# Performance work log

Hardware: AMD Instinct MI355X
Metric: run time of the kernel (lower is better)

## Reference

```python
import jax, jax.numpy as jnp
import numpy as np

SPLIT_SHAPE = (16, 16, 16, 16)  # per-variable state counts; joint space = 65536
NUM_CLASSES = 100
STABLE = 1e-6


def setup_inputs() -> dict:
    key = jax.random.key(0)
    k1, k2 = jax.random.split(key)
    B = 1024
    logits = jax.random.normal(k1, (B, sum(SPLIT_SHAPE)), dtype=jnp.float32)
    labels = jax.random.randint(k2, (B,), 0, NUM_CLASSES)
    y_true = jax.nn.one_hot(labels, NUM_CLASSES, dtype=jnp.float32)
    return {"logits": logits, "y_true": y_true}


def reference(logits, y_true):
    B = logits.shape[0]
    # split logits into per-variable blocks and softmax each -> P(Ak|Xi)
    splits = np.cumsum(SPLIT_SHAPE)[:-1]
    variables = [jax.nn.softmax(p, axis=-1) for p in jnp.split(logits, splits, axis=-1)]
    # joint sample space via iterative outer products: [B, s1, ..., sN]
    joint = variables[0]
    for v in variables[1:]:
        joint = jnp.einsum('b...,ba->b...a', joint, v)
    flat = joint.reshape(B, -1)  # [B, J], J = prod(SPLIT_SHAPE)
    # observation: numerator/denominator counts (fresh recorder, first call)
    num_y_joint = jnp.einsum('bj,by->yj', flat, y_true)  # [Y, J]
    num_joint = jnp.sum(flat, axis=0)                     # [J]
    prob_y_joint = jnp.clip(
        jnp.maximum(num_y_joint, STABLE) / jnp.maximum(num_joint, STABLE), 0.0, 1.0)
    # inference: posterior P^A(Yi|Xi)
    probs = jnp.einsum('yj,bj->by', prob_y_joint, flat)  # [B, Y]
    return probs
```

## Files before the change

### kernel.cpp

```cpp
#include <hip/hip_runtime.h>
#include <hip/hip_bf16.h>

#define EPS 1e-6f

typedef float f32x4 __attribute__((ext_vector_type(4)));
typedef __bf16 bf16x8 __attribute__((ext_vector_type(8)));
typedef short short8 __attribute__((ext_vector_type(8)));

static __device__ __forceinline__ short bf16bits(float x) {
    __hip_bfloat16 h = __float2bfloat16(x);
    short s;
    __builtin_memcpy(&s, &h, 2);
    return s;
}
static __device__ __forceinline__ void bsplit(float x, short& h, short& l) {
    __hip_bfloat16 hb = __float2bfloat16(x);
    __builtin_memcpy(&h, &hb, 2);
    float hf = __bfloat162float(hb);
    __hip_bfloat16 lb = __float2bfloat16(x - hf);
    __builtin_memcpy(&l, &lb, 2);
}

static __device__ __forceinline__ bf16x8 gload16(const short* p) {
    bf16x8 r;
    asm volatile("global_load_dwordx4 %0, %1, off"
                 : "=&v"(r) : "v"(p) : "memory");
    return r;
}
#define WAITV(N)                                                   \
    do {                                                           \
        asm volatile("s_waitcnt vmcnt(" #N ")" ::: "memory");      \
        __builtin_amdgcn_sched_barrier(0);                         \
    } while (0)

__global__ __launch_bounds__(256) void kA(const float* __restrict__ logits,
                                          const float* __restrict__ y_true,
                                          float* __restrict__ P23,
                                          float* __restrict__ P01T,
                                          short* __restrict__ P23s_hi,
                                          int* __restrict__ label) {
    __shared__ float row[64];
    int b = blockIdx.x, t = threadIdx.x;
    if (t < 64) {
        float x = logits[b * 64 + t];
        float m = x;
        for (int mk = 8; mk >= 1; mk >>= 1) m = fmaxf(m, __shfl_xor(m, mk, 16));
        float e = __expf(x - m);
        float s = e;
        for (int mk = 8; mk >= 1; mk >>= 1) s += __shfl_xor(s, mk, 16);
        row[t] = e / s;
    }
    if (t >= 128 && t < 228) {
        int y = t - 128;
        if (y_true[b * 100 + y] > 0.5f) label[b] = y;
    }
    __syncthreads();
    int hi = t >> 4, lo = t & 15;
    float v01 = row[hi] * row[16 + lo];
    float v23 = row[32 + hi] * row[48 + lo];
    P01T[t * 1024 + b] = v01;
    P23[b * 256 + t] = v23;
    int ts = t ^ ((b & 7) << 3);
    P23s_hi[b * 256 + ts] = bf16bits(v23);
}

__global__ __launch_bounds__(1024) void kS(const int* __restrict__ label,
                                           int* __restrict__ bidx,
                                           int* __restrict__ off_g,
                                           float* __restrict__ numjoint) {
    __shared__ int lab[1024];
    __shared__ unsigned bm[101 * 32];
    __shared__ int hist[101];
    __shared__ int offs[101];
    int t = threadIdx.x;
    for (int i = t; i < 65536; i += 1024) numjoint[i] = 0.f;
    lab[t] = label[t];
    if (t < 101) hist[t] = 0;
    for (int i = t; i < 101 * 32; i += 1024) bm[i] = 0u;
    __syncthreads();
    int my = lab[t];
    atomicAdd(&hist[my], 1);
    atomicOr(&bm[my * 32 + (t >> 5)], 1u << (t & 31));
    __syncthreads();
    if (t == 0) {
        int s = 0;
        for (int y = 0; y < 101; ++y) { offs[y] = s; s += hist[y]; }
    }
    __syncthreads();
    int w = t >> 5;
    int rank = 0;
    for (int i = 0; i < w; ++i) rank += __popc(bm[my * 32 + i]);
    rank += __popc(bm[my * 32 + w] & ((1u << (t & 31)) - 1u));
    bidx[offs[my] + rank] = t;
    if (t <= 100) off_g[t] = offs[t];
}

__global__ __launch_bounds__(256) void kP(const float* __restrict__ P23,
                                          const float* __restrict__ P01T,
                                          const int* __restrict__ bidx,
                                          float* __restrict__ P23sort,
                                          float* __restrict__ P01Ts) {
    int bid = blockIdx.x, t = threadIdx.x;
    if (bid < 1024) {
        P23sort[bid * 256 + t] = P23[bidx[bid] * 256 + t];
    } else {
        int u = bid - 1024;
        for (int i = t; i < 1024; i += 256)
            P01Ts[u * 1024 + i] = P01T[u * 1024 + bidx[i]];
    }
}

__global__ __launch_bounds__(256, 4) void kNJ(const float* __restrict__ P01Ts,
                                              const float* __restrict__ P23sort,
                                              float* __restrict__ numjoint) {
    __shared__ short Bh[4 * 64 * 8];
    __shared__ short Bl[4 * 64 * 8];
    int t = threadIdx.x;
    int bid = blockIdx.x;
    int ub = (bid & 3) << 6;
    int tb = ((bid >> 2) & 3) << 6;
    int koff = (bid >> 4) << 6;
    int lane = t & 63, w = t >> 6;
    int l15 = lane & 15, l4 = lane >> 4;

    const float* pa = P01Ts + (size_t)(ub + w * 16 + l15) * 1024 + koff + (l4 << 3);
    int sr = t >> 3, sc = (t & 7) << 3;

    const f32x4 zero4 = {0.f, 0.f, 0.f, 0.f};
    f32x4 acc0 = zero4, acc1 = zero4, acc2 = zero4, acc3 = zero4;

    #pragma unroll
    for (int kc = 0; kc < 2; ++kc) {
        __syncthreads();
        {
            const float* pb = P23sort + (size_t)(koff + kc * 32 + sr) * 256 + tb + sc;
            #pragma unroll
            for (int q = 0; q < 8; ++q) {
                short h, l;
                bsplit(pb[q], h, l);
                int tcl = sc + q;
                int ad = (((tcl >> 4) << 6) + (tcl & 15) + ((sr >> 3) << 4)) * 8 + (sr & 7);
                Bh[ad] = h; Bl[ad] = l;
            }
        }
        __syncthreads();
        union { short8 s; bf16x8 b; } Ah, Al;
        #pragma unroll
        for (int q = 0; q < 8; ++q) {
            short h, l;
            bsplit(pa[kc * 32 + q], h, l);
            Ah.s[q] = h; Al.s[q] = l;
        }
        {
            bf16x8 bh0 = *(const bf16x8*)(Bh + (lane) * 8);
            bf16x8 bl0 = *(const bf16x8*)(Bl + (lane) * 8);
            bf16x8 bh1 = *(const bf16x8*)(Bh + (64 + lane) * 8);
            bf16x8 bl1 = *(const bf16x8*)(Bl + (64 + lane) * 8);
            bf16x8 bh2 = *(const bf16x8*)(Bh + (128 + lane) * 8);
            bf16x8 bl2 = *(const bf16x8*)(Bl + (128 + lane) * 8);
            bf16x8 bh3 = *(const bf16x8*)(Bh + (192 + lane) * 8);
            bf16x8 bl3 = *(const bf16x8*)(Bl + (192 + lane) * 8);
            acc0 = __builtin_amdgcn_mfma_f32_16x16x32_bf16(Ah.b, bh0, acc0, 0, 0, 0);
            acc0 = __builtin_amdgcn_mfma_f32_16x16x32_bf16(Ah.b, bl0, acc0, 0, 0, 0);
            acc0 = __builtin_amdgcn_mfma_f32_16x16x32_bf16(Al.b, bh0, acc0, 0, 0, 0);
            acc1 = __builtin_amdgcn_mfma_f32_16x16x32_bf16(Ah.b, bh1, acc1, 0, 0, 0);
            acc1 = __builtin_amdgcn_mfma_f32_16x16x32_bf16(Ah.b, bl1, acc1, 0, 0, 0);
            acc1 = __builtin_amdgcn_mfma_f32_16x16x32_bf16(Al.b, bh1, acc1, 0, 0, 0);
            acc2 = __builtin_amdgcn_mfma_f32_16x16x32_bf16(Ah.b, bh2, acc2, 0, 0, 0);
            acc2 = __builtin_amdgcn_mfma_f32_16x16x32_bf16(Ah.b, bl2, acc2, 0, 0, 0);
            acc2 = __builtin_amdgcn_mfma_f32_16x16x32_bf16(Al.b, bh2, acc2, 0, 0, 0);
            acc3 = __builtin_amdgcn_mfma_f32_16x16x32_bf16(Ah.b, bh3, acc3, 0, 0, 0);
            acc3 = __builtin_amdgcn_mfma_f32_16x16x32_bf16(Ah.b, bl3, acc3, 0, 0, 0);
            acc3 = __builtin_amdgcn_mfma_f32_16x16x32_bf16(Al.b, bh3, acc3, 0, 0, 0);
        }
    }
    #pragma unroll
    for (int n = 0; n < 4; ++n) {
        f32x4 a = (n == 0) ? acc0 : (n == 1) ? acc1 : (n == 2) ? acc2 : acc3;
        #pragma unroll
        for (int r = 0; r < 4; ++r) {
            int u = ub + w * 16 + (l4 << 2) + r;
            int tc = tb + (n << 4) + l15;
            atomicAdd(&numjoint[u * 256 + tc], a[r]);
        }
    }
}

__global__ __launch_bounds__(256, 2) void kY(const float* __restrict__ P01Ts,
                                             const float* __restrict__ P23sort,
                                             const int* __restrict__ off_g,
                                             const float* __restrict__ numjoint,
                                             short* __restrict__ pyF) {
    __shared__ short Bh[8 * 64 * 8];
    __shared__ short Bl[8 * 64 * 8];
    __shared__ short ct[4][16 * 128];
    int y = blockIdx.x >> 1;
    int th = blockIdx.x & 1;
    int t = threadIdx.x;
    int lane = t & 63, w = t >> 6;
    int l15 = lane & 15, l4 = lane >> 4;
    int yt = y >> 4, yl = y & 15;

    if (y >= 100) {
        short8 z = {0, 0, 0, 0, 0, 0, 0, 0};
        #pragma unroll
        for (int ut = 0; ut < 4; ++ut)
            #pragma unroll
            for (int rep = 0; rep < 4; ++rep) {
                int c = (rep << 6) + lane;
                int ul = c >> 4, t8 = (c & 15) << 3;
                int u = (w << 6) + (ut << 4) + ul;
                int j0 = u * 256 + (th << 7) + t8;
                size_t sa = ((size_t)((j0 >> 5) * 8 + yt) * 64 + yl + (((j0 >> 3) & 3) << 4)) * 8;
                *(short8*)(pyF + sa) = z;
            }
        return;
    }

    int off = off_g[y];
    int n = off_g[y + 1] - off;
    int nk = (n + 31) >> 5;

    const f32x4 zero4 = {0.f, 0.f, 0.f, 0.f};
    f32x4 acc[4][8];
    #pragma unroll
    for (int a = 0; a < 4; ++a)
        #pragma unroll
        for (int b = 0; b < 8; ++b) acc[a][b] = zero4;

    int sr = t >> 3, sc = (t & 7) << 3;
    const float* paw = P01Ts + (size_t)((w << 6) + l15) * 1024 + off + (l4 << 3);

    #pragma unroll 1
    for (int kc = 0; kc < nk; ++kc) {
        __syncthreads();
        #pragma unroll
        for (int rep = 0; rep < 2; ++rep) {
            int tl0 = (rep << 6) + sc;
            int row = kc * 32 + sr;
            float vals[8];
            if (row < n) {
                const float* pb = P23sort + (size_t)(off + row) * 256 + (th << 7) + tl0;
                #pragma unroll
                for (int q = 0; q < 8; ++q) vals[q] = pb[q];
            } else {
                #pragma unroll
                for (int q = 0; q < 8; ++q) vals[q] = 0.f;
            }
            #pragma unroll
            for (int q = 0; q < 8; ++q) {
                short h, l;
                bsplit(vals[q], h, l);
                int tl = tl0 + q;
                int ad = (((tl >> 4) << 6) + (tl & 15) + ((sr >> 3) << 4)) * 8 + (sr & 7);
                Bh[ad] = h; Bl[ad] = l;
            }
        }
        __syncthreads();
        #pragma unroll
        for (int ut = 0; ut < 4; ++ut) {
            union { short8 s; bf16x8 b; } Ah, Al;
            #pragma unroll
            for (int q = 0; q < 8; ++q) {
                short h, l;
                bsplit(paw[(size_t)ut * 16384 + kc * 32 + q], h, l);
                Ah.s[q] = h; Al.s[q] = l;
            }
            #pragma unroll
            for (int tt = 0; tt < 8; ++tt) {
                bf16x8 bh = *(const bf16x8*)(Bh + ((tt << 6) + lane) * 8);
                bf16x8 bl = *(const bf16x8*)(Bl + ((tt << 6) + lane) * 8);
                acc[ut][tt] = __builtin_amdgcn_mfma_f32_16x16x32_bf16(Ah.b, bh, acc[ut][tt], 0, 0, 0);
                acc[ut][tt] = __builtin_amdgcn_mfma_f32_16x16x32_bf16(Ah.b, bl, acc[ut][tt], 0, 0, 0);
                acc[ut][tt] = __builtin_amdgcn_mfma_f32_16x16x32_bf16(Al.b, bh, acc[ut][tt], 0, 0, 0);
            }
        }
    }

    #pragma unroll
    for (int ut = 0; ut < 4; ++ut) {
        #pragma unroll
        for (int tt = 0; tt < 8; ++tt) {
            #pragma unroll
            for (int r = 0; r < 4; ++r) {
                int u = (w << 6) + (ut << 4) + (l4 << 2) + r;
                int tg = (th << 7) + (tt << 4) + l15;
                float nj = numjoint[u * 256 + tg];
                float q = fminf(fmaxf(acc[ut][tt][r], EPS) / fmaxf(nj, EPS), 1.0f);
                ct[w][((l4 << 2) + r) * 128 + (tt << 4) + l15] = bf16bits(q);
            }
        }
        asm volatile("s_waitcnt lgkmcnt(0)" ::: "memory");
        __builtin_amdgcn_sched_barrier(0);
        #pragma unroll
        for (int rep = 0; rep < 4; ++rep) {
            int c = (rep << 6) + lane;
            int ul = c >> 4, t8 = (c & 15) << 3;
            short8 v = *(const short8*)(ct[w] + ul * 128 + t8);
            int u = (w << 6) + (ut << 4) + ul;
            int j0 = u * 256 + (th << 7) + t8;
            size_t sa = ((size_t)((j0 >> 5) * 8 + yt) * 64 + yl + (((j0 >> 3) & 3) << 4)) * 8;
            *(short8*)(pyF + sa) = v;
        }
        asm volatile("s_waitcnt lgkmcnt(0)" ::: "memory");
        __builtin_amdgcn_sched_barrier(0);
    }
}

__global__ __launch_bounds__(512, 2) void kC(const short* __restrict__ P23s_hi,
                                             const float* __restrict__ P01T,
                                             const short* __restrict__ pyF,
                                             float* __restrict__ part) {
    __shared__ short Ahi[64 * 256];
    __shared__ float p01s[8 * 64];
    int t = threadIdx.x;
    int bb = blockIdx.x >> 5, uspl = blockIdx.x & 31;
    int bbase = bb << 6;
    int u0 = uspl << 3;

    #pragma unroll
    for (int r = 0; r < 4; ++r) {
        int c = r * 512 + t;
        *(short8*)(Ahi + c * 8) = *(const short8*)(P23s_hi + bbase * 256 + c * 8);
    }
    p01s[t] = P01T[(u0 + (t >> 6)) * 1024 + bbase + (t & 63)];
    __syncthreads();

    int lane = t & 63;
    int wave = t >> 6;
    int wb = wave >> 2, wy = wave & 3;
    int l15 = lane & 15, l4 = lane >> 4;
    int hi8 = l4 << 3;

    int rowA0 = wb * 32 + l15;
    int swz = (rowA0 & 7) << 3;
    const short* pA0h = Ahi + rowA0 * 256;
    const short* pA1h = pA0h + 16 * 256;

    const short* pf = pyF + (size_t)(uspl * 64 * 8 + wy * 2) * 512 + lane * 8;
    int y0 = wy * 32 + l15;

    const f32x4 zero4 = {0.f, 0.f, 0.f, 0.f};
    f32x4 P00 = zero4, P01v = zero4, P10 = zero4, P11 = zero4;
    bf16x8 W0, W1, X0, X1, Y0, Y1, Z0, Z1;

#define COMPUTE(CUR0, CUR1, KS)                                                  \
    {                                                                            \
        int aoff = ((KS) * 32 + hi8) ^ swz;                                      \
        bf16x8 a0h = *(const bf16x8*)(pA0h + aoff);                              \
        bf16x8 a1h = *(const bf16x8*)(pA1h + aoff);                              \
        f32x4 c00 = ((KS) == 0) ? zero4 : Q00;                                   \
        f32x4 c01 = ((KS) == 0) ? zero4 : Q01;                                   \
        f32x4 c10 = ((KS) == 0) ? zero4 : Q10;                                   \
        f32x4 c11 = ((KS) == 0) ? zero4 : Q11;                                   \
        c00 = __builtin_amdgcn_mfma_f32_16x16x32_bf16(a0h, CUR0, c00, 0, 0, 0);  \
        c10 = __builtin_amdgcn_mfma_f32_16x16x32_bf16(a1h, CUR0, c10, 0, 0, 0);  \
        c01 = __builtin_amdgcn_mfma_f32_16x16x32_bf16(a0h, CUR1, c01, 0, 0, 0);  \
        c11 = __builtin_amdgcn_mfma_f32_16x16x32_bf16(a1h, CUR1, c11, 0, 0, 0);  \
        Q00 = c00; Q01 = c01; Q10 = c10; Q11 = c11;                              \
    }
#define STEP(CUR0, CUR1, NXT0, NXT1, KS, S3)    \
    NXT0 = gload16(pf + (S3) * 4096);           \
    NXT1 = gload16(pf + (S3) * 4096 + 512);     \
    WAITV(6);                                   \
    COMPUTE(CUR0, CUR1, KS)

    {
        W0 = gload16(pf);        W1 = gload16(pf + 512);
        X0 = gload16(pf + 4096); X1 = gload16(pf + 4096 + 512);
        Y0 = gload16(pf + 8192); Y1 = gload16(pf + 8192 + 512);
    }

    #pragma unroll 1
    for (int uu = 0; uu < 7; ++uu) {
        int s0 = uu * 8;
        f32x4 Q00, Q01, Q10, Q11;
        STEP(W0, W1, Z0, Z1, 0, s0 + 3)
        STEP(X0, X1, W0, W1, 1, s0 + 4)
        STEP(Y0, Y1, X0, X1, 2, s0 + 5)
        STEP(Z0, Z1, Y0, Y1, 3, s0 + 6)
        STEP(W0, W1, Z0, Z1, 4, s0 + 7)
        STEP(X0, X1, W0, W1, 5, s0 + 8)
        STEP(Y0, Y1, X0, X1, 6, s0 + 9)
        STEP(Z0, Z1, Y0, Y1, 7, s0 + 10)
        f32x4 pv0 = *(const f32x4*)(p01s + uu * 64 + wb * 32 + (l4 << 2));
        f32x4 pv1 = *(const f32x4*)(p01s + uu * 64 + wb * 32 + 16 + (l4 << 2));
        P00 += pv0 * Q00; P01v += pv0 * Q01;
        P10 += pv1 * Q10; P11 += pv1 * Q11;
    }
    {
        f32x4 Q00, Q01, Q10, Q11;
        STEP(W0, W1, Z0, Z1, 0, 59)
        STEP(X0, X1, W0, W1, 1, 60)
        STEP(Y0, Y1, X0, X1, 2, 61)
        STEP(Z0, Z1, Y0, Y1, 3, 62)
        STEP(W0, W1, Z0, Z1, 4, 63)
        WAITV(4); COMPUTE(X0, X1, 5)
        WAITV(2); COMPUTE(Y0, Y1, 6)
        WAITV(0); COMPUTE(Z0, Z1, 7)
        f32x4 pv0 = *(const f32x4*)(p01s + 7 * 64 + wb * 32 + (l4 << 2));
        f32x4 pv1 = *(const f32x4*)(p01s + 7 * 64 + wb * 32 + 16 + (l4 << 2));
        P00 += pv0 * Q00; P01v += pv0 * Q01;
        P10 += pv1 * Q10; P11 += pv1 * Q11;
    }
#undef STEP
#undef COMPUTE

    size_t pbase = (size_t)uspl * 128 * 1024;
    {
        int bg0 = bbase + wb * 32 + (l4 << 2);
        int bg1 = bg0 + 16;
        *(f32x4*)(part + pbase + (size_t)y0 * 1024 + bg0) = P00;
        *(f32x4*)(part + pbase + (size_t)y0 * 1024 + bg1) = P10;
        *(f32x4*)(part + pbase + (size_t)(y0 + 16) * 1024 + bg0) = P01v;
        *(f32x4*)(part + pbase + (size_t)(y0 + 16) * 1024 + bg1) = P11;
    }
}

__global__ __launch_bounds__(256) void kD(const float* __restrict__ part,
                                          float* __restrict__ out) {
    int t = threadIdx.x;
    int y = blockIdx.x >> 2;
    int b = ((blockIdx.x & 3) << 8) + t;
    float s = 0.f;
    for (int q = 0; q < 32; ++q)
        s += part[(((size_t)q * 128 + y) << 10) + b];
    out[(size_t)b * 100 + y] = s;
}

extern "C" void kernel_launch(void* const* d_in, const int* in_sizes, int n_in,
                              void* d_out, int out_size, void* d_ws, size_t ws_size,
                              hipStream_t stream) {
    const float* logits = (const float*)d_in[0];
    const float* y_true = (const float*)d_in[1];
    float* out = (float*)d_out;

    char* ws = (char*)d_ws;
    float* P23      = (float*)(ws + (1u << 20));
    float* P01T     = (float*)(ws + (2u << 20));
    short* P23s_hi  = (short*)(ws + (3u << 20));
    int*   lab      = (int*)(ws + (4u << 20));
    int*   bidx     = (int*)(ws + (4u << 20) + 4096);
    int*   off_g    = (int*)(ws + (4u << 20) + 8192);
    float* P23sort  = (float*)(ws + (5u << 20));
    float* P01Ts    = (float*)(ws + (6u << 20));
    short* pyF      = (short*)(ws + (8u << 20));
    float* numjoint = (float*)(ws + (24u << 20));
    float* part     = (float*)(ws + (40u << 20));

    kA<<<1024, 256, 0, stream>>>(logits, y_true, P23, P01T, P23s_hi, lab);
    kS<<<1, 1024, 0, stream>>>(lab, bidx, off_g, numjoint);
    kP<<<1280, 256, 0, stream>>>(P23, P01T, bidx, P23sort, P01Ts);
    kNJ<<<256, 256, 0, stream>>>(P01Ts, P23sort, numjoint);
    kY<<<256, 256, 0, stream>>>(P01Ts, P23sort, off_g, numjoint, pyF);
    kC<<<512, 512, 0, stream>>>(P23s_hi, P01T, pyF, part);
    kD<<<400, 256, 0, stream>>>(part, out);
}
```

Measured before the change: 82.18 us.

## Fuse label sort into numjoint kernel and gather unsorted rows in kY

Removes the separate single-block sort kernel and the permutation kernel. The sort becomes an extra block of the numjoint GEMM kernel, and numjoint zeroing moves into kA. The numjoint GEMM now reads the unsorted P01T/P23, since a sum over the batch does not depend on order. kY gathers rows through bidx into a shared staging buffer instead of reading pre-permuted copies. This cuts two launches and a full permutation pass, at the cost of extra shared memory and indirect loads in kY.

```diff
diff --git a/kernel.cpp b/kernel.cpp
--- a/kernel.cpp
+++ b/kernel.cpp
@@ -36,9 +36,11 @@
 __global__ __launch_bounds__(256) void kA(const float* __restrict__ logits,
                                           const float* __restrict__ y_true,
                                           float* __restrict__ P23,
+                                          float* __restrict__ P01,
                                           float* __restrict__ P01T,
                                           short* __restrict__ P23s_hi,
-                                          int* __restrict__ label) {
+                                          int* __restrict__ label,
+                                          float* __restrict__ numjoint) {
     __shared__ float row[64];
     int b = blockIdx.x, t = threadIdx.x;
     if (t < 64) {
@@ -54,76 +56,69 @@
         int y = t - 128;
         if (y_true[b * 100 + y] > 0.5f) label[b] = y;
     }
+    if (t < 64) numjoint[b * 64 + t] = 0.f;
     __syncthreads();
     int hi = t >> 4, lo = t & 15;
     float v01 = row[hi] * row[16 + lo];
     float v23 = row[32 + hi] * row[48 + lo];
+    P01[b * 256 + t] = v01;
     P01T[t * 1024 + b] = v01;
     P23[b * 256 + t] = v23;
     int ts = t ^ ((b & 7) << 3);
     P23s_hi[b * 256 + ts] = bf16bits(v23);
 }
 
-__global__ __launch_bounds__(1024) void kS(const int* __restrict__ label,
-                                           int* __restrict__ bidx,
-                                           int* __restrict__ off_g,
-                                           float* __restrict__ numjoint) {
-    __shared__ int lab[1024];
-    __shared__ unsigned bm[101 * 32];
-    __shared__ int hist[101];
-    __shared__ int offs[101];
+__global__ __launch_bounds__(256, 4) void kSNJ(const float* __restrict__ P01T,
+                                               const float* __restrict__ P23,
+                                               const int* __restrict__ label,
+                                               int* __restrict__ bidx,
+                                               int* __restrict__ off_g,
+                                               float* __restrict__ numjoint) {
     int t = threadIdx.x;
-    for (int i = t; i < 65536; i += 1024) numjoint[i] = 0.f;
-    lab[t] = label[t];
-    if (t < 101) hist[t] = 0;
-    for (int i = t; i < 101 * 32; i += 1024) bm[i] = 0u;
-    __syncthreads();
-    int my = lab[t];
-    atomicAdd(&hist[my], 1);
-    atomicOr(&bm[my * 32 + (t >> 5)], 1u << (t & 31));
-    __syncthreads();
-    if (t == 0) {
-        int s = 0;
-        for (int y = 0; y < 101; ++y) { offs[y] = s; s += hist[y]; }
-    }
-    __syncthreads();
-    int w = t >> 5;
-    int rank = 0;
-    for (int i = 0; i < w; ++i) rank += __popc(bm[my * 32 + i]);
-    rank += __popc(bm[my * 32 + w] & ((1u << (t & 31)) - 1u));
-    bidx[offs[my] + rank] = t;
-    if (t <= 100) off_g[t] = offs[t];
-}
-
-__global__ __launch_bounds__(256) void kP(const float* __restrict__ P23,
-                                          const float* __restrict__ P01T,
-                                          const int* __restrict__ bidx,
-                                          float* __restrict__ P23sort,
-                                          float* __restrict__ P01Ts) {
-    int bid = blockIdx.x, t = threadIdx.x;
-    if (bid < 1024) {
-        P23sort[bid * 256 + t] = P23[bidx[bid] * 256 + t];
-    } else {
-        int u = bid - 1024;
-        for (int i = t; i < 1024; i += 256)
-            P01Ts[u * 1024 + i] = P01T[u * 1024 + bidx[i]];
-    }
-}
-
-__global__ __launch_bounds__(256, 4) void kNJ(const float* __restrict__ P01Ts,
-                                              const float* __restrict__ P23sort,
-                                              float* __restrict__ numjoint) {
+    int bid = blockIdx.x;
+
+    if (bid == 256) {
+        __shared__ int lab[1024];
+        __shared__ unsigned bm[101 * 32];
+        __shared__ int hist[101];
+        __shared__ int offs[101];
+        for (int i = t; i < 1024; i += 256) lab[i] = label[i];
+        if (t < 101) hist[t] = 0;
+        for (int i = t; i < 101 * 32; i += 256) bm[i] = 0u;
+        __syncthreads();
+        for (int i = t; i < 1024; i += 256) {
+            int my = lab[i];
+            atomicAdd(&hist[my], 1);
+            atomicOr(&bm[my * 32 + (i >> 5)], 1u << (i & 31));
+        }
+        __syncthreads();
+        if (t == 0) {
+            int s = 0;
+            for (int y = 0; y < 101; ++y) { offs[y] = s; s += hist[y]; }
+        }
+        __syncthreads();
+        for (int i = t; i < 1024; i += 256) {
+            int my = lab[i];
+            int w = i >> 5;
+            int rank = 0;
+            for (int q = 0; q < 32; ++q)
+                if (q < w) rank += __popc(bm[my * 32 + q]);
+            rank += __popc(bm[my * 32 + w] & ((1u << (i & 31)) - 1u));
+            bidx[offs[my] + rank] = i;
+        }
+        if (t <= 100) off_g[t] = offs[t];
+        return;
+    }
+
     __shared__ short Bh[4 * 64 * 8];
     __shared__ short Bl[4 * 64 * 8];
-    int t = threadIdx.x;
-    int bid = blockIdx.x;
     int ub = (bid & 3) << 6;
     int tb = ((bid >> 2) & 3) << 6;
     int koff = (bid >> 4) << 6;
     int lane = t & 63, w = t >> 6;
     int l15 = lane & 15, l4 = lane >> 4;
 
-    const float* pa = P01Ts + (size_t)(ub + w * 16 + l15) * 1024 + koff + (l4 << 3);
+    const float* pa = P01T + (size_t)(ub + w * 16 + l15) * 1024 + koff + (l4 << 3);
     int sr = t >> 3, sc = (t & 7) << 3;
 
     const f32x4 zero4 = {0.f, 0.f, 0.f, 0.f};
@@ -133,7 +128,7 @@
     for (int kc = 0; kc < 2; ++kc) {
         __syncthreads();
         {
-            const float* pb = P23sort + (size_t)(koff + kc * 32 + sr) * 256 + tb + sc;
+            const float* pb = P23 + (size_t)(koff + kc * 32 + sr) * 256 + tb + sc;
             #pragma unroll
             for (int q = 0; q < 8; ++q) {
                 short h, l;
@@ -186,14 +181,17 @@
     }
 }
 
-__global__ __launch_bounds__(256, 2) void kY(const float* __restrict__ P01Ts,
-                                             const float* __restrict__ P23sort,
+__global__ __launch_bounds__(256, 2) void kY(const float* __restrict__ P01,
+                                             const float* __restrict__ P23,
+                                             const int* __restrict__ bidx,
                                              const int* __restrict__ off_g,
                                              const float* __restrict__ numjoint,
                                              short* __restrict__ pyF) {
     __shared__ short Bh[8 * 64 * 8];
     __shared__ short Bl[8 * 64 * 8];
     __shared__ short ct[4][16 * 128];
+    __shared__ float aStage[32][258];
+    __shared__ int sbidx[32];
     int y = blockIdx.x >> 1;
     int th = blockIdx.x & 1;
     int t = threadIdx.x;
@@ -229,18 +227,24 @@
         for (int b = 0; b < 8; ++b) acc[a][b] = zero4;
 
     int sr = t >> 3, sc = (t & 7) << 3;
-    const float* paw = P01Ts + (size_t)((w << 6) + l15) * 1024 + off + (l4 << 3);
 
     #pragma unroll 1
     for (int kc = 0; kc < nk; ++kc) {
         __syncthreads();
+        if (t < 32) {
+            int idx = off + kc * 32 + t;
+            sbidx[t] = bidx[(idx < 1024) ? idx : 1023];
+        }
+        __syncthreads();
+        for (int it = 0; it < 32; ++it)
+            aStage[it][t] = P01[sbidx[it] * 256 + t];
         #pragma unroll
         for (int rep = 0; rep < 2; ++rep) {
             int tl0 = (rep << 6) + sc;
             int row = kc * 32 + sr;
             float vals[8];
             if (row < n) {
-                const float* pb = P23sort + (size_t)(off + row) * 256 + (th << 7) + tl0;
+                const float* pb = P23 + (size_t)sbidx[sr] * 256 + (th << 7) + tl0;
                 #pragma unroll
                 for (int q = 0; q < 8; ++q) vals[q] = pb[q];
             } else {
@@ -263,7 +267,7 @@
             #pragma unroll
             for (int q = 0; q < 8; ++q) {
                 short h, l;
-                bsplit(paw[(size_t)ut * 16384 + kc * 32 + q], h, l);
+                bsplit(aStage[(l4 << 3) + q][(w << 6) + (ut << 4) + l15], h, l);
                 Ah.s[q] = h; Al.s[q] = l;
             }
             #pragma unroll
@@ -436,23 +440,20 @@
     float* out = (float*)d_out;
 
     char* ws = (char*)d_ws;
+    float* P01      = (float*)(ws);
     float* P23      = (float*)(ws + (1u << 20));
     float* P01T     = (float*)(ws + (2u << 20));
     short* P23s_hi  = (short*)(ws + (3u << 20));
     int*   lab      = (int*)(ws + (4u << 20));
     int*   bidx     = (int*)(ws + (4u << 20) + 4096);
     int*   off_g    = (int*)(ws + (4u << 20) + 8192);
-    float* P23sort  = (float*)(ws + (5u << 20));
-    float* P01Ts    = (float*)(ws + (6u << 20));
     short* pyF      = (short*)(ws + (8u << 20));
     float* numjoint = (float*)(ws + (24u << 20));
     float* part     = (float*)(ws + (40u << 20));
 
-    kA<<<1024, 256, 0, stream>>>(logits, y_true, P23, P01T, P23s_hi, lab);
-    kS<<<1, 1024, 0, stream>>>(lab, bidx, off_g, numjoint);
-    kP<<<1280, 256, 0, stream>>>(P23, P01T, bidx, P23sort, P01Ts);
-    kNJ<<<256, 256, 0, stream>>>(P01Ts, P23sort, numjoint);
-    kY<<<256, 256, 0, stream>>>(P01Ts, P23sort, off_g, numjoint, pyF);
+    kA<<<1024, 256, 0, stream>>>(logits, y_true, P23, P01, P01T, P23s_hi, lab, numjoint);
+    kSNJ<<<257, 256, 0, stream>>>(P01T, P23, lab, bidx, off_g, numjoint);
+    kY<<<256, 256, 0, stream>>>(P01, P23, bidx, off_g, numjoint, pyF);
     kC<<<512, 512, 0, stream>>>(P23s_hi, P01T, pyF, part);
     kD<<<400, 256, 0, stream>>>(part, out);
 }
```

After: 75.95 us. 1.08x faster.
